# Performance work log

Hardware: AMD Instinct MI355X
Metric: run time of the kernel (lower is better)

The kernel has to match this reference:

```python
import jax, jax.numpy as jnp
import numpy as np

N_NODES = 50000
E_RAW = 1600000
EMB_DIM = 32
HID = 128
OUT = 128


def setup_inputs() -> dict:
    key = jax.random.key(0)
    k1, k2, k3, k4, k5, k6 = jax.random.split(key, 6)
    x = jnp.arange(N_NODES, dtype=jnp.int64)
    edge_index = jax.random.randint(k1, (2, E_RAW), 0, N_NODES, dtype=jnp.int64)
    emb = jax.random.normal(k2, (N_NODES, EMB_DIM), dtype=jnp.float32)
    W1 = jax.random.normal(k3, (EMB_DIM, HID), dtype=jnp.float32) / np.sqrt(EMB_DIM)
    b1 = jnp.zeros((HID,), dtype=jnp.float32)
    W2 = jax.random.normal(k4, (HID, OUT), dtype=jnp.float32) / np.sqrt(HID)
    b2 = jnp.zeros((OUT,), dtype=jnp.float32)
    return {"x": x, "edge_index": edge_index, "emb": emb,
            "W1": W1, "b1": b1, "W2": W2, "b2": b2}


def _gcn_norm(edge_index, num_nodes):
    # add self-loops, then symmetric normalization deg^-1/2 A_hat deg^-1/2
    loop = jnp.arange(num_nodes, dtype=edge_index.dtype)
    src = jnp.concatenate([edge_index[0], loop])
    dst = jnp.concatenate([edge_index[1], loop])
    ones = jnp.ones(src.shape[0], dtype=jnp.float32)
    deg = jax.ops.segment_sum(ones, dst, num_segments=num_nodes)
    dinv = jax.lax.rsqrt(deg)  # deg >= 1 due to self-loops
    norm = dinv[src] * dinv[dst]  # [E+N]
    return src, dst, norm


def _gcn_conv(h, src, dst, norm, W, b, num_nodes):
    h = h @ W                                  # [N, d_out] dense GEMM
    msg = h[src] * norm[:, None]               # gather + edge scale
    agg = jax.ops.segment_sum(msg, dst, num_segments=num_nodes)  # scatter-add
    return agg + b


def reference(x, edge_index, emb, W1, b1, W2, b2):
    num_nodes = emb.shape[0]
    h = emb[x]                                 # embedding lookup
    src, dst, norm = _gcn_norm(edge_index, num_nodes)
    h = _gcn_conv(h, src, dst, norm, W1, b1, num_nodes)
    h = jax.nn.relu(h)
    out = _gcn_conv(h, src, dst, norm, W2, b2, num_nodes)
    return out
```

## Files before the change

kernel.cpp:

```cpp
#include <hip/hip_runtime.h>


#define NPP   6250
#define NC    32

static inline int cdiv(int a, int b){ return (a + b - 1) / b; }

__device__ __forceinline__ unsigned short f2bf(float f){
    unsigned int u = __float_as_uint(f);
    u += 0x7fffu + ((u >> 16) & 1u);
    return (unsigned short)(u >> 16);
}
__device__ __forceinline__ float bf2f(unsigned short b){
    return __uint_as_float(((unsigned int)b) << 16);
}

__global__ void k_zero_i32(int* __restrict__ p, int n){
    int i = blockIdx.x * blockDim.x + threadIdx.x;
    if (i < n) p[i] = 0;
}

__global__ __launch_bounds__(256) void k_bucket(const int* __restrict__ src,
        const int* __restrict__ dst, int E, int* __restrict__ staged_s,
        int* __restrict__ staged_d, int* __restrict__ gcur, int npp, int C){
    __shared__ int  qcnt[8];
    __shared__ int  qbase[8];
    __shared__ int2 qbuf[8 * 256];
    int tid = threadIdx.x;
    if (tid < 8) qcnt[tid] = 0;
    __syncthreads();
    int e0 = blockIdx.x * 1024 + tid * 4;
    if (e0 + 3 < E){
        int4 d4 = *(const int4*)(dst + e0);
        int4 s4 = *(const int4*)(src + e0);
        int dd[4] = {d4.x, d4.y, d4.z, d4.w};
        int ss[4] = {s4.x, s4.y, s4.z, s4.w};
        #pragma unroll
        for (int i = 0; i < 4; i++){
            int p = dd[i] / npp;
            int pos = atomicAdd(&qcnt[p], 1);
            if (pos < 256) qbuf[p * 256 + pos] = make_int2(ss[i], dd[i]);
            else {
                int gp = atomicAdd(&gcur[p], 1);
                staged_s[(size_t)p * C + gp] = ss[i];
                staged_d[(size_t)p * C + gp] = dd[i];
            }
        }
    } else {
        for (int e = e0; e < E && e < e0 + 4; e++){
            int d = dst[e], s = src[e];
            int p = d / npp;
            int pos = atomicAdd(&qcnt[p], 1);
            if (pos < 256) qbuf[p * 256 + pos] = make_int2(s, d);
            else {
                int gp = atomicAdd(&gcur[p], 1);
                staged_s[(size_t)p * C + gp] = s;
                staged_d[(size_t)p * C + gp] = d;
            }
        }
    }
    __syncthreads();
    if (tid < 8){
        int nq = min(qcnt[tid], 256);
        qbase[tid] = (nq > 0) ? atomicAdd(&gcur[tid], nq) : 0;
    }
    __syncthreads();
    for (int b = 0; b < 8; b++){
        int nq = min(qcnt[b], 256);
        int gb = qbase[b];
        for (int i = tid; i < nq; i += 256){
            int2 pr = qbuf[b * 256 + i];
            staged_s[(size_t)b * C + gb + i] = pr.x;
            staged_d[(size_t)b * C + gb + i] = pr.y;
        }
    }
}

__global__ __launch_bounds__(256) void k_hist(const int* __restrict__ staged_d,
        const int* __restrict__ gcur, int C, int CH, int npp, int* __restrict__ H){
    __shared__ int hist[NPP];
    int part  = blockIdx.x & 7;
    int chunk = blockIdx.x >> 3;
    int tid = threadIdx.x;
    for (int i = tid; i < npp; i += 256) hist[i] = 0;
    __syncthreads();
    int pc = gcur[part];
    int lo = part * npp;
    int e0 = chunk * CH, e1 = min(e0 + CH, pc);
    const int* sd = staged_d + (size_t)part * C;
    for (int e = e0 + tid; e < e1; e += 256)
        atomicAdd(&hist[sd[e] - lo], 1);
    __syncthreads();
    int* Hrow = H + (size_t)(part * NC + chunk) * npp;
    for (int i = tid; i < npp; i += 256) Hrow[i] = hist[i];
}

__global__ __launch_bounds__(256) void k_nodescan(int* __restrict__ H, int npp, int n,
        int* __restrict__ ecount, float* __restrict__ dinv){
    int t = blockIdx.x * blockDim.x + threadIdx.x;
    if (t >= 8 * npp) return;
    int p  = t / npp;
    int dl = t - p * npp;
    int d  = p * npp + dl;
    if (d >= n) return;
    int run = 0;
    #pragma unroll
    for (int c = 0; c < NC; c++){
        size_t idx = (size_t)(p * NC + c) * npp + dl;
        int v = H[idx];
        H[idx] = run;
        run += v;
    }
    ecount[d] = run;
    dinv[d] = rsqrtf((float)run + 1.0f);
}

__global__ void k_scanA(const int* __restrict__ ecount, int n, int* __restrict__ bsum){
    __shared__ int s[256];
    int t = threadIdx.x;
    int i = blockIdx.x * 256 + t;
    s[t] = (i < n) ? ecount[i] : 0;
    __syncthreads();
    for (int d = 128; d > 0; d >>= 1){
        if (t < d) s[t] += s[t + d];
        __syncthreads();
    }
    if (t == 0) bsum[blockIdx.x] = s[0];
}

__global__ void k_scanB(int* __restrict__ bsum, int nb){
    __shared__ int s[256];
    int t = threadIdx.x;
    s[t] = (t < nb) ? bsum[t] : 0;
    __syncthreads();
    if (t == 0){
        int run = 0;
        for (int b = 0; b < nb; b++){ int v = s[b]; s[b] = run; run += v; }
    }
    __syncthreads();
    if (t < nb) bsum[t] = s[t];
}

__global__ void k_scanC(const int* __restrict__ ecount, int n, const int* __restrict__ bsum,
                        int* __restrict__ offsets){
    __shared__ int s[256];
    int t = threadIdx.x;
    int i = blockIdx.x * 256 + t;
    int v = (i < n) ? ecount[i] : 0;
    s[t] = v;
    __syncthreads();
    for (int d = 1; d < 256; d <<= 1){
        int x = (t >= d) ? s[t - d] : 0;
        __syncthreads();
        s[t] += x;
        __syncthreads();
    }
    if (i < n) offsets[i] = bsum[blockIdx.x] + s[t] - v;
}

__global__ __launch_bounds__(256) void k_fill3(const int* __restrict__ staged_s,
        const int* __restrict__ staged_d, const int* __restrict__ gcur, int C, int CH,
        int npp, const int* __restrict__ H, const int* __restrict__ offsets,
        int* __restrict__ csr_src){
    __shared__ int cur[NPP];
    int part  = blockIdx.x & 7;
    int chunk = blockIdx.x >> 3;
    int tid = threadIdx.x;
    const int* Hrow = H + (size_t)(part * NC + chunk) * npp;
    for (int i = tid; i < npp; i += 256) cur[i] = Hrow[i];
    __syncthreads();
    int pc = gcur[part];
    int lo = part * npp;
    int e0 = chunk * CH, e1 = min(e0 + CH, pc);
    const int* ss = staged_s + (size_t)part * C;
    const int* sd = staged_d + (size_t)part * C;
    for (int e = e0 + tid; e < e1; e += 256){
        int d = sd[e];
        int r = atomicAdd(&cur[d - lo], 1);
        csr_src[offsets[d] + r] = ss[e];
    }
}

__global__ void k_scale(const float* __restrict__ emb, const int* __restrict__ x,
                        const float* __restrict__ dinv, unsigned short* __restrict__ es, int n){
    int idx = blockIdx.x * blockDim.x + threadIdx.x;
    if (idx >= n * 32) return;
    int i = idx >> 5;
    int c = idx & 31;
    es[idx] = f2bf(emb[(size_t)x[i] * 32 + c] * dinv[i]);
}

__global__ __launch_bounds__(256) void k_agg32(const unsigned short* __restrict__ es,
        const int* __restrict__ offsets, const int* __restrict__ ecount,
        const int* __restrict__ csr, const float* __restrict__ dinv,
        float* __restrict__ a1, int n){
    int node = blockIdx.x * 8 + (threadIdx.x >> 5);
    int lane = threadIdx.x & 31;
    if (node >= n) return;
    int off = offsets[node], cnt = ecount[node];
    float s0 = bf2f(es[(size_t)node * 32 + lane]);
    float s1 = 0.f;
    int e = 0;
    for (; e + 8 <= cnt; e += 8){
        int i0 = csr[off + e + 0], i1 = csr[off + e + 1];
        int i2 = csr[off + e + 2], i3 = csr[off + e + 3];
        int i4 = csr[off + e + 4], i5 = csr[off + e + 5];
        int i6 = csr[off + e + 6], i7 = csr[off + e + 7];
        unsigned short v0 = es[(size_t)i0 * 32 + lane];
        unsigned short v1 = es[(size_t)i1 * 32 + lane];
        unsigned short v2 = es[(size_t)i2 * 32 + lane];
        unsigned short v3 = es[(size_t)i3 * 32 + lane];
        unsigned short v4 = es[(size_t)i4 * 32 + lane];
        unsigned short v5 = es[(size_t)i5 * 32 + lane];
        unsigned short v6 = es[(size_t)i6 * 32 + lane];
        unsigned short v7 = es[(size_t)i7 * 32 + lane];
        s0 += bf2f(v0) + bf2f(v2) + bf2f(v4) + bf2f(v6);
        s1 += bf2f(v1) + bf2f(v3) + bf2f(v5) + bf2f(v7);
    }
    for (; e < cnt; e++) s0 += bf2f(es[(size_t)csr[off + e] * 32 + lane]);
    a1[(size_t)node * 32 + lane] = dinv[node] * (s0 + s1);
}

__global__ __launch_bounds__(256) void k_mlp1(const float* __restrict__ a1,
        const float* __restrict__ W1, const float* __restrict__ b1,
        const float* __restrict__ dinv, unsigned short* __restrict__ hs, int n){
    __shared__ float w[32 * 128];
    for (int i = threadIdx.x; i < 32 * 128; i += 256) w[i] = W1[i];
    __syncthreads();
    int c4  = (threadIdx.x & 31) * 4;
    int row = blockIdx.x * 8 + (threadIdx.x >> 5);
    if (row >= n) return;
    const float4* ar = (const float4*)(a1 + (size_t)row * 32);
    float4 acc = *(const float4*)(b1 + c4);
    #pragma unroll
    for (int k4 = 0; k4 < 8; k4++){
        float4 av = ar[k4];
        float4 w0 = *(const float4*)&w[(k4 * 4 + 0) * 128 + c4];
        float4 w1 = *(const float4*)&w[(k4 * 4 + 1) * 128 + c4];
        float4 w2 = *(const float4*)&w[(k4 * 4 + 2) * 128 + c4];
        float4 w3 = *(const float4*)&w[(k4 * 4 + 3) * 128 + c4];
        acc.x += av.x * w0.x + av.y * w1.x + av.z * w2.x + av.w * w3.x;
        acc.y += av.x * w0.y + av.y * w1.y + av.z * w2.y + av.w * w3.y;
        acc.z += av.x * w0.z + av.y * w1.z + av.z * w2.z + av.w * w3.z;
        acc.w += av.x * w0.w + av.y * w1.w + av.z * w2.w + av.w * w3.w;
    }
    float dv = dinv[row];
    ushort4 o;
    o.x = f2bf(dv * fmaxf(acc.x, 0.f));
    o.y = f2bf(dv * fmaxf(acc.y, 0.f));
    o.z = f2bf(dv * fmaxf(acc.z, 0.f));
    o.w = f2bf(dv * fmaxf(acc.w, 0.f));
    *(ushort4*)(hs + (size_t)row * 128 + c4) = o;
}

__global__ __launch_bounds__(256) void k_agg128(const unsigned short* __restrict__ hs,
        const int* __restrict__ offsets, const int* __restrict__ ecount,
        const int* __restrict__ csr, const float* __restrict__ dinv,
        float* __restrict__ a2, int n){
    int node = blockIdx.x * 8 + (threadIdx.x >> 5);
    int lane = threadIdx.x & 31;
    if (node >= n) return;
    int off = offsets[node], cnt = ecount[node];
    int c4 = lane * 4;
    ushort4 sv = *(const ushort4*)(hs + (size_t)node * 128 + c4);
    float ax0 = bf2f(sv.x), ax1 = 0.f;
    float ay0 = bf2f(sv.y), ay1 = 0.f;
    float az0 = bf2f(sv.z), az1 = 0.f;
    float aw0 = bf2f(sv.w), aw1 = 0.f;
    int e = 0;
    for (; e + 8 <= cnt; e += 8){
        int i0 = csr[off + e + 0], i1 = csr[off + e + 1];
        int i2 = csr[off + e + 2], i3 = csr[off + e + 3];
        int i4 = csr[off + e + 4], i5 = csr[off + e + 5];
        int i6 = csr[off + e + 6], i7 = csr[off + e + 7];
        ushort4 v0 = *(const ushort4*)(hs + (size_t)i0 * 128 + c4);
        ushort4 v1 = *(const ushort4*)(hs + (size_t)i1 * 128 + c4);
        ushort4 v2 = *(const ushort4*)(hs + (size_t)i2 * 128 + c4);
        ushort4 v3 = *(const ushort4*)(hs + (size_t)i3 * 128 + c4);
        ushort4 v4 = *(const ushort4*)(hs + (size_t)i4 * 128 + c4);
        ushort4 v5 = *(const ushort4*)(hs + (size_t)i5 * 128 + c4);
        ushort4 v6 = *(const ushort4*)(hs + (size_t)i6 * 128 + c4);
        ushort4 v7 = *(const ushort4*)(hs + (size_t)i7 * 128 + c4);
        ax0 += bf2f(v0.x) + bf2f(v2.x) + bf2f(v4.x) + bf2f(v6.x);
        ax1 += bf2f(v1.x) + bf2f(v3.x) + bf2f(v5.x) + bf2f(v7.x);
        ay0 += bf2f(v0.y) + bf2f(v2.y) + bf2f(v4.y) + bf2f(v6.y);
        ay1 += bf2f(v1.y) + bf2f(v3.y) + bf2f(v5.y) + bf2f(v7.y);
        az0 += bf2f(v0.z) + bf2f(v2.z) + bf2f(v4.z) + bf2f(v6.z);
        az1 += bf2f(v1.z) + bf2f(v3.z) + bf2f(v5.z) + bf2f(v7.z);
        aw0 += bf2f(v0.w) + bf2f(v2.w) + bf2f(v4.w) + bf2f(v6.w);
        aw1 += bf2f(v1.w) + bf2f(v3.w) + bf2f(v5.w) + bf2f(v7.w);
    }
    for (; e < cnt; e++){
        ushort4 v = *(const ushort4*)(hs + (size_t)csr[off + e] * 128 + c4);
        ax0 += bf2f(v.x); ay0 += bf2f(v.y); az0 += bf2f(v.z); aw0 += bf2f(v.w);
    }
    float dv = dinv[node];
    float4 r;
    r.x = dv * (ax0 + ax1); r.y = dv * (ay0 + ay1);
    r.z = dv * (az0 + az1); r.w = dv * (aw0 + aw1);
    *(float4*)(a2 + (size_t)node * 128 + c4) = r;
}

#define MLP2_STEP(KK, COMP) {                                        \
    float4 wv = *(const float4*)&w[(k + KK) * 64 + c4];              \
    acc0.x += a0.COMP * wv.x; acc0.y += a0.COMP * wv.y;              \
    acc0.z += a0.COMP * wv.z; acc0.w += a0.COMP * wv.w;              \
    acc1.x += a1v.COMP * wv.x; acc1.y += a1v.COMP * wv.y;            \
    acc1.z += a1v.COMP * wv.z; acc1.w += a1v.COMP * wv.w;            \
    acc2.x += a2v.COMP * wv.x; acc2.y += a2v.COMP * wv.y;            \
    acc2.z += a2v.COMP * wv.z; acc2.w += a2v.COMP * wv.w;            \
    acc3.x += a3v.COMP * wv.x; acc3.y += a3v.COMP * wv.y;            \
    acc3.z += a3v.COMP * wv.z; acc3.w += a3v.COMP * wv.w; }

__global__ __launch_bounds__(256) void k_mlp2(const float* __restrict__ a2,
        const float* __restrict__ W2, const float* __restrict__ b2,
        float* __restrict__ out, int n){
    __shared__ float w[128 * 64];
    int half  = blockIdx.x & 1;
    int rb    = blockIdx.x >> 1;
    int cbase = half * 64;
    for (int i = threadIdx.x; i < 128 * 16; i += 256){
        int k = i >> 4, c = (i & 15) * 4;
        *(float4*)&w[k * 64 + c] = *(const float4*)(W2 + (size_t)k * 128 + cbase + c);
    }
    __syncthreads();
    int c4 = (threadIdx.x & 15) * 4;
    int r0 = rb * 64 + (threadIdx.x >> 4) * 4;
    float4 bias = *(const float4*)(b2 + cbase + c4);
    float4 acc0 = bias, acc1 = bias, acc2 = bias, acc3 = bias;
    const float* h0 = a2 + (size_t)min(r0 + 0, n - 1) * 128;
    const float* h1 = a2 + (size_t)min(r0 + 1, n - 1) * 128;
    const float* h2 = a2 + (size_t)min(r0 + 2, n - 1) * 128;
    const float* h3 = a2 + (size_t)min(r0 + 3, n - 1) * 128;
    for (int k = 0; k < 128; k += 4){
        float4 a0  = *(const float4*)(h0 + k);
        float4 a1v = *(const float4*)(h1 + k);
        float4 a2v = *(const float4*)(h2 + k);
        float4 a3v = *(const float4*)(h3 + k);
        MLP2_STEP(0, x)
        MLP2_STEP(1, y)
        MLP2_STEP(2, z)
        MLP2_STEP(3, w)
    }
    if (r0 + 0 < n) *(float4*)(out + (size_t)(r0 + 0) * 128 + cbase + c4) = acc0;
    if (r0 + 1 < n) *(float4*)(out + (size_t)(r0 + 1) * 128 + cbase + c4) = acc1;
    if (r0 + 2 < n) *(float4*)(out + (size_t)(r0 + 2) * 128 + cbase + c4) = acc2;
    if (r0 + 3 < n) *(float4*)(out + (size_t)(r0 + 3) * 128 + cbase + c4) = acc3;
}

extern "C" void kernel_launch(void* const* d_in, const int* in_sizes, int n_in,
                              void* d_out, int out_size, void* d_ws, size_t ws_size,
                              hipStream_t stream){
    const int*   x    = (const int*)d_in[0];
    const int*   ei   = (const int*)d_in[1];
    const float* emb  = (const float*)d_in[2];
    const float* W1   = (const float*)d_in[3];
    const float* b1   = (const float*)d_in[4];
    const float* W2   = (const float*)d_in[5];
    const float* b2   = (const float*)d_in[6];
    const int N = in_sizes[0];
    const int E = in_sizes[1] / 2;
    const int* srcv = ei;
    const int* dstv = ei + E;
    float* out = (float*)d_out;

    char* p = (char*)d_ws;
    auto alloc = [&](size_t bytes) -> char* {
        char* r = p; p += (bytes + 255) & ~(size_t)255; return r;
    };
    int nb = cdiv(N, 256);
    int*            ecount  = (int*)           alloc((size_t)(N + 8) * 4);
    int*            gcur    = ecount + N;
    int*            offsets = (int*)           alloc((size_t)N * 4);
    int*            bsum    = (int*)           alloc((size_t)nb * 4);
    float*          dinv    = (float*)         alloc((size_t)N * 4);
    int*            csr     = (int*)           alloc((size_t)E * 4);
    unsigned short* es      = (unsigned short*)alloc((size_t)N * 32 * 2);
    float*          a1      = (float*)         alloc((size_t)N * 32 * 4);
    unsigned short* hs      = (unsigned short*)alloc((size_t)N * 128 * 2);
    float*          a2      = (float*)         alloc((size_t)N * 128 * 4);
    (void)ws_size; (void)n_in; (void)out_size;

    const int npp = cdiv(N, 8);
    const int C   = E / 8 + 65536;
    const int CH  = cdiv(C, NC);
    int* staged_s = (int*)a2;
    int* staged_d = staged_s + (size_t)8 * C;
    int* H = (int*)es;

    k_zero_i32<<<1, 64, 0, stream>>>(gcur, 8);
    k_bucket  <<<cdiv(E, 1024), 256, 0, stream>>>(srcv, dstv, E, staged_s, staged_d, gcur, npp, C);
    k_hist    <<<8 * NC, 256, 0, stream>>>(staged_d, gcur, C, CH, npp, H);
    k_nodescan<<<cdiv(8 * npp, 256), 256, 0, stream>>>(H, npp, N, ecount, dinv);
    k_scanA   <<<nb, 256, 0, stream>>>(ecount, N, bsum);
    k_scanB   <<<1, 256, 0, stream>>>(bsum, nb);
    k_scanC   <<<nb, 256, 0, stream>>>(ecount, N, bsum, offsets);
    k_fill3   <<<8 * NC, 256, 0, stream>>>(staged_s, staged_d, gcur, C, CH, npp, H, offsets, csr);

    k_scale <<<cdiv(N * 32, 256), 256, 0, stream>>>(emb, x, dinv, es, N);
    k_agg32 <<<cdiv(N, 8), 256, 0, stream>>>(es, offsets, ecount, csr, dinv, a1, N);
    k_mlp1  <<<cdiv(N, 8), 256, 0, stream>>>(a1, W1, b1, dinv, hs, N);

    k_agg128<<<cdiv(N, 8), 256, 0, stream>>>(hs, offsets, ecount, csr, dinv, a2, N);
    k_mlp2  <<<cdiv(N, 64) * 2, 256, 0, stream>>>(a2, W2, b2, out, N);
}
```

Measured before the change: 291.4 us.

## Split 128-wide aggregation into four 32-column slabs and fuse scan kernels

The hidden features are now written by k_mlp1 into four column-slab arrays of 32 bf16 each. The second aggregation runs as four launches, each gathering one slab, so each gathered working set (about 3.2 MB) is more likely to stay in cache across random neighbor reads. The degree scan is merged into k_nodescan (block sums) and a combined k_scanBC, which removes two launches. CSR index loads now use nontemporal hints. The cost is reading the CSR indices four times and three extra kernel launches for aggregation.

```diff
diff --git a/kernel.cpp b/kernel.cpp
--- a/kernel.cpp
+++ b/kernel.cpp
@@ -96,55 +96,44 @@
 }
 
 __global__ __launch_bounds__(256) void k_nodescan(int* __restrict__ H, int npp, int n,
-        int* __restrict__ ecount, float* __restrict__ dinv){
-    int t = blockIdx.x * blockDim.x + threadIdx.x;
-    if (t >= 8 * npp) return;
-    int p  = t / npp;
-    int dl = t - p * npp;
-    int d  = p * npp + dl;
-    if (d >= n) return;
+        int* __restrict__ ecount, float* __restrict__ dinv, int* __restrict__ bsum){
+    __shared__ int s[256];
+    int t = blockIdx.x * 256 + threadIdx.x;
     int run = 0;
-    #pragma unroll
-    for (int c = 0; c < NC; c++){
-        size_t idx = (size_t)(p * NC + c) * npp + dl;
-        int v = H[idx];
-        H[idx] = run;
-        run += v;
-    }
-    ecount[d] = run;
-    dinv[d] = rsqrtf((float)run + 1.0f);
-}
-
-__global__ void k_scanA(const int* __restrict__ ecount, int n, int* __restrict__ bsum){
+    if (t < 8 * npp && t < n){
+        int p  = t / npp;
+        int dl = t - p * npp;
+        #pragma unroll
+        for (int c = 0; c < NC; c++){
+            size_t idx = (size_t)(p * NC + c) * npp + dl;
+            int v = H[idx];
+            H[idx] = run;
+            run += v;
+        }
+        ecount[t] = run;
+        dinv[t] = rsqrtf((float)run + 1.0f);
+    }
+    s[threadIdx.x] = run;
+    __syncthreads();
+    for (int d = 128; d > 0; d >>= 1){
+        if (threadIdx.x < d) s[threadIdx.x] += s[threadIdx.x + d];
+        __syncthreads();
+    }
+    if (threadIdx.x == 0) bsum[blockIdx.x] = s[0];
+}
+
+__global__ __launch_bounds__(256) void k_scanBC(const int* __restrict__ ecount, int n,
+        const int* __restrict__ bsum, int nb, int* __restrict__ offsets){
+    __shared__ int bs[256];
     __shared__ int s[256];
     int t = threadIdx.x;
-    int i = blockIdx.x * 256 + t;
-    s[t] = (i < n) ? ecount[i] : 0;
-    __syncthreads();
-    for (int d = 128; d > 0; d >>= 1){
-        if (t < d) s[t] += s[t + d];
-        __syncthreads();
-    }
-    if (t == 0) bsum[blockIdx.x] = s[0];
-}
-
-__global__ void k_scanB(int* __restrict__ bsum, int nb){
-    __shared__ int s[256];
-    int t = threadIdx.x;
-    s[t] = (t < nb) ? bsum[t] : 0;
+    bs[t] = (t < nb) ? bsum[t] : 0;
     __syncthreads();
     if (t == 0){
         int run = 0;
-        for (int b = 0; b < nb; b++){ int v = s[b]; s[b] = run; run += v; }
-    }
-    __syncthreads();
-    if (t < nb) bsum[t] = s[t];
-}
-
-__global__ void k_scanC(const int* __restrict__ ecount, int n, const int* __restrict__ bsum,
-                        int* __restrict__ offsets){
-    __shared__ int s[256];
-    int t = threadIdx.x;
+        for (int b = 0; b < nb; b++){ int v = bs[b]; bs[b] = run; run += v; }
+    }
+    __syncthreads();
     int i = blockIdx.x * 256 + t;
     int v = (i < n) ? ecount[i] : 0;
     s[t] = v;
@@ -155,7 +144,7 @@
         s[t] += x;
         __syncthreads();
     }
-    if (i < n) offsets[i] = bsum[blockIdx.x] + s[t] - v;
+    if (i < n) offsets[i] = bs[blockIdx.x] + s[t] - v;
 }
 
 __global__ __launch_bounds__(256) void k_fill3(const int* __restrict__ staged_s,
@@ -202,10 +191,14 @@
     float s1 = 0.f;
     int e = 0;
     for (; e + 8 <= cnt; e += 8){
-        int i0 = csr[off + e + 0], i1 = csr[off + e + 1];
-        int i2 = csr[off + e + 2], i3 = csr[off + e + 3];
-        int i4 = csr[off + e + 4], i5 = csr[off + e + 5];
-        int i6 = csr[off + e + 6], i7 = csr[off + e + 7];
+        int i0 = __builtin_nontemporal_load(csr + off + e + 0);
+        int i1 = __builtin_nontemporal_load(csr + off + e + 1);
+        int i2 = __builtin_nontemporal_load(csr + off + e + 2);
+        int i3 = __builtin_nontemporal_load(csr + off + e + 3);
+        int i4 = __builtin_nontemporal_load(csr + off + e + 4);
+        int i5 = __builtin_nontemporal_load(csr + off + e + 5);
+        int i6 = __builtin_nontemporal_load(csr + off + e + 6);
+        int i7 = __builtin_nontemporal_load(csr + off + e + 7);
         unsigned short v0 = es[(size_t)i0 * 32 + lane];
         unsigned short v1 = es[(size_t)i1 * 32 + lane];
         unsigned short v2 = es[(size_t)i2 * 32 + lane];
@@ -250,37 +243,42 @@
     o.y = f2bf(dv * fmaxf(acc.y, 0.f));
     o.z = f2bf(dv * fmaxf(acc.z, 0.f));
     o.w = f2bf(dv * fmaxf(acc.w, 0.f));
-    *(ushort4*)(hs + (size_t)row * 128 + c4) = o;
-}
-
-__global__ __launch_bounds__(256) void k_agg128(const unsigned short* __restrict__ hs,
+    int q   = c4 >> 5;
+    int c32 = c4 & 31;
+    *(ushort4*)(hs + (size_t)q * n * 32 + (size_t)row * 32 + c32) = o;
+}
+
+__global__ __launch_bounds__(256) void k_agg128q(const unsigned short* __restrict__ slab,
         const int* __restrict__ offsets, const int* __restrict__ ecount,
         const int* __restrict__ csr, const float* __restrict__ dinv,
-        float* __restrict__ a2, int n){
-    int node = blockIdx.x * 8 + (threadIdx.x >> 5);
-    int lane = threadIdx.x & 31;
+        float* __restrict__ a2, int n, int cb){
+    int node = blockIdx.x * 32 + (threadIdx.x >> 3);
+    int l4 = (threadIdx.x & 7) * 4;
     if (node >= n) return;
     int off = offsets[node], cnt = ecount[node];
-    int c4 = lane * 4;
-    ushort4 sv = *(const ushort4*)(hs + (size_t)node * 128 + c4);
+    ushort4 sv = *(const ushort4*)(slab + (size_t)node * 32 + l4);
     float ax0 = bf2f(sv.x), ax1 = 0.f;
     float ay0 = bf2f(sv.y), ay1 = 0.f;
     float az0 = bf2f(sv.z), az1 = 0.f;
     float aw0 = bf2f(sv.w), aw1 = 0.f;
     int e = 0;
     for (; e + 8 <= cnt; e += 8){
-        int i0 = csr[off + e + 0], i1 = csr[off + e + 1];
-        int i2 = csr[off + e + 2], i3 = csr[off + e + 3];
-        int i4 = csr[off + e + 4], i5 = csr[off + e + 5];
-        int i6 = csr[off + e + 6], i7 = csr[off + e + 7];
-        ushort4 v0 = *(const ushort4*)(hs + (size_t)i0 * 128 + c4);
-        ushort4 v1 = *(const ushort4*)(hs + (size_t)i1 * 128 + c4);
-        ushort4 v2 = *(const ushort4*)(hs + (size_t)i2 * 128 + c4);
-        ushort4 v3 = *(const ushort4*)(hs + (size_t)i3 * 128 + c4);
-        ushort4 v4 = *(const ushort4*)(hs + (size_t)i4 * 128 + c4);
-        ushort4 v5 = *(const ushort4*)(hs + (size_t)i5 * 128 + c4);
-        ushort4 v6 = *(const ushort4*)(hs + (size_t)i6 * 128 + c4);
-        ushort4 v7 = *(const ushort4*)(hs + (size_t)i7 * 128 + c4);
+        int i0 = __builtin_nontemporal_load(csr + off + e + 0);
+        int i1 = __builtin_nontemporal_load(csr + off + e + 1);
+        int i2 = __builtin_nontemporal_load(csr + off + e + 2);
+        int i3 = __builtin_nontemporal_load(csr + off + e + 3);
+        int i4 = __builtin_nontemporal_load(csr + off + e + 4);
+        int i5 = __builtin_nontemporal_load(csr + off + e + 5);
+        int i6 = __builtin_nontemporal_load(csr + off + e + 6);
+        int i7 = __builtin_nontemporal_load(csr + off + e + 7);
+        ushort4 v0 = *(const ushort4*)(slab + (size_t)i0 * 32 + l4);
+        ushort4 v1 = *(const ushort4*)(slab + (size_t)i1 * 32 + l4);
+        ushort4 v2 = *(const ushort4*)(slab + (size_t)i2 * 32 + l4);
+        ushort4 v3 = *(const ushort4*)(slab + (size_t)i3 * 32 + l4);
+        ushort4 v4 = *(const ushort4*)(slab + (size_t)i4 * 32 + l4);
+        ushort4 v5 = *(const ushort4*)(slab + (size_t)i5 * 32 + l4);
+        ushort4 v6 = *(const ushort4*)(slab + (size_t)i6 * 32 + l4);
+        ushort4 v7 = *(const ushort4*)(slab + (size_t)i7 * 32 + l4);
         ax0 += bf2f(v0.x) + bf2f(v2.x) + bf2f(v4.x) + bf2f(v6.x);
         ax1 += bf2f(v1.x) + bf2f(v3.x) + bf2f(v5.x) + bf2f(v7.x);
         ay0 += bf2f(v0.y) + bf2f(v2.y) + bf2f(v4.y) + bf2f(v6.y);
@@ -291,14 +289,14 @@
         aw1 += bf2f(v1.w) + bf2f(v3.w) + bf2f(v5.w) + bf2f(v7.w);
     }
     for (; e < cnt; e++){
-        ushort4 v = *(const ushort4*)(hs + (size_t)csr[off + e] * 128 + c4);
+        ushort4 v = *(const ushort4*)(slab + (size_t)csr[off + e] * 32 + l4);
         ax0 += bf2f(v.x); ay0 += bf2f(v.y); az0 += bf2f(v.z); aw0 += bf2f(v.w);
     }
     float dv = dinv[node];
     float4 r;
     r.x = dv * (ax0 + ax1); r.y = dv * (ay0 + ay1);
     r.z = dv * (az0 + az1); r.w = dv * (aw0 + aw1);
-    *(float4*)(a2 + (size_t)node * 128 + c4) = r;
+    *(float4*)(a2 + (size_t)node * 128 + cb + l4) = r;
 }
 
 #define MLP2_STEP(KK, COMP) {                                        \
@@ -391,16 +389,17 @@
     k_zero_i32<<<1, 64, 0, stream>>>(gcur, 8);
     k_bucket  <<<cdiv(E, 1024), 256, 0, stream>>>(srcv, dstv, E, staged_s, staged_d, gcur, npp, C);
     k_hist    <<<8 * NC, 256, 0, stream>>>(staged_d, gcur, C, CH, npp, H);
-    k_nodescan<<<cdiv(8 * npp, 256), 256, 0, stream>>>(H, npp, N, ecount, dinv);
-    k_scanA   <<<nb, 256, 0, stream>>>(ecount, N, bsum);
-    k_scanB   <<<1, 256, 0, stream>>>(bsum, nb);
-    k_scanC   <<<nb, 256, 0, stream>>>(ecount, N, bsum, offsets);
+    k_nodescan<<<nb, 256, 0, stream>>>(H, npp, N, ecount, dinv, bsum);
+    k_scanBC  <<<nb, 256, 0, stream>>>(ecount, N, bsum, nb, offsets);
     k_fill3   <<<8 * NC, 256, 0, stream>>>(staged_s, staged_d, gcur, C, CH, npp, H, offsets, csr);
 
     k_scale <<<cdiv(N * 32, 256), 256, 0, stream>>>(emb, x, dinv, es, N);
     k_agg32 <<<cdiv(N, 8), 256, 0, stream>>>(es, offsets, ecount, csr, dinv, a1, N);
     k_mlp1  <<<cdiv(N, 8), 256, 0, stream>>>(a1, W1, b1, dinv, hs, N);
 
-    k_agg128<<<cdiv(N, 8), 256, 0, stream>>>(hs, offsets, ecount, csr, dinv, a2, N);
+    for (int q = 0; q < 4; q++){
+        k_agg128q<<<cdiv(N, 32), 256, 0, stream>>>(hs + (size_t)q * N * 32,
+                offsets, ecount, csr, dinv, a2, N, q * 32);
+    }
     k_mlp2  <<<cdiv(N, 64) * 2, 256, 0, stream>>>(a2, W2, b2, out, N);
 }
```

After: 336.9 us. +15.6%, slower.
